# Kernel tuning notes

Hardware: AMD Instinct MI355X
Metric: run time of the kernel (lower is better)

## Reference

```python
import jax, jax.numpy as jnp
import numpy as np

EPS = 1e-12  # matches torch F.normalize default eps

def _l2_normalize(x):
    n = jnp.maximum(jnp.linalg.norm(x, axis=-1, keepdims=True), EPS)
    return x / n

def setup_inputs() -> dict:
    key = jax.random.key(0)
    ks = jax.random.split(key, 6)
    B, H, N, D, E = 4, 12, 4096, 64, 32
    Q = jax.random.normal(ks[0], (B, H, N, D), dtype=jnp.float32)
    K = jax.random.normal(ks[1], (B, H, N, D), dtype=jnp.float32)
    we = jax.random.normal(ks[2], (2, H, D, E), dtype=jnp.float32)
    wr = jax.random.normal(ks[3], (2, H, D, E), dtype=jnp.float32)
    mask = jnp.ones((B, N), dtype=jnp.float32)
    W = jax.random.normal(ks[4], (D, 2 * E), dtype=jnp.float32) * (1.0 / np.sqrt(2 * E))
    b = jnp.zeros((D,), dtype=jnp.float32)
    Lambda = jax.random.uniform(ks[5], (H, E), dtype=jnp.float32)
    return {"Q": Q, "K": K, "we": we, "wr": wr, "mask": mask, "W": W, "b": b, "Lambda": Lambda}

def reference(Q, K, we, wr, mask, W, b, Lambda):
    # feature map: L2 normalize along head_dim
    queries = _l2_normalize(Q)   # [B,H,N,D]
    keys = _l2_normalize(K)      # [B,H,N,D]
    # per-head low-rank projections
    escore = jnp.einsum('bhnd,hde->bhne', queries, we[0])  # [B,H,N,E]
    rscore = jnp.einsum('bhnd,hde->bhne', keys, wr[0])     # [B,H,N,E]
    score = jnp.concatenate([escore, rscore], axis=-1)      # [B,H,N,2E]
    # Linear(2E -> D): score @ W.T + b
    attn_out = jnp.einsum('bhne,de->bhnd', score, W) + b
    attn_out = attn_out * mask[:, None, :, None]
    # trace_no_x = False branch
    return (attn_out, escore, rscore, we[0], wr[0], queries, keys, Lambda)
```

## Files before the change

kernel.cpp:

```cpp
#include <hip/hip_runtime.h>


namespace {
constexpr int Hh = 12;
constexpr int Nn = 4096;
constexpr int Dd = 64;
constexpr int O_ATTN = 0;
constexpr int O_ES   = 12582912;
constexpr int O_RS   = 18874368;
constexpr int O_WE   = 25165824;
constexpr int O_WR   = 25190400;
constexpr int O_Q    = 25214976;
constexpr int O_K    = 37797888;
constexpr int O_LAM  = 50380800;
}

__device__ __forceinline__ int aswz(int d, int r) {
    return d * 128 + (r ^ ((d & 7) << 2));
}

__global__ __launch_bounds__(256, 3)
void pca_fused(const float* __restrict__ Q, const float* __restrict__ Kp,
               const float* __restrict__ we, const float* __restrict__ wr,
               const float* __restrict__ mask, const float* __restrict__ W,
               const float* __restrict__ bias, const float* __restrict__ Lam,
               float* __restrict__ out)
{
    __shared__ float lds[12288];
    float* A  = lds;
    float* Bs = lds + 8192;

    const int tid = threadIdx.x;
    const int bh  = blockIdx.x >> 6;
    const int n0  = (blockIdx.x & 63) << 6;
    const int h   = bh % Hh;
    const int bb  = bh / Hh;

    if (blockIdx.x < 49) {
        int i4 = blockIdx.x * 256 + tid;
        if (i4 < 6144) {
            ((float4*)(out + O_WE))[i4] = ((const float4*)we)[i4];
        } else if (i4 < 12288) {
            ((float4*)(out + O_WR))[i4 - 6144] = ((const float4*)wr)[i4 - 6144];
        } else if (i4 < 12384) {
            ((float4*)(out + O_LAM))[i4 - 12288] = ((const float4*)Lam)[i4 - 12288];
        }
    }

    float wreg[16];
#pragma unroll
    for (int j = 0; j < 16; ++j) wreg[j] = W[tid + 256 * j];

    {
        const float* weh = we + h * 2048;
        const float* wrh = wr + h * 2048;
#pragma unroll
        for (int j = 0; j < 8; ++j) {
            int i = tid + 256 * j;
            int d = i >> 5, e = i & 31;
            Bs[d * 64 + e]      = weh[i];
            Bs[d * 64 + 32 + e] = wrh[i];
        }
    }
    {
        const int rr = tid >> 4;
        const int c4 = (tid & 15) << 2;
#pragma unroll
        for (int p = 0; p < 4; ++p) {
            int r = p * 16 + rr;
            int g = (bh * Nn + n0 + r) * Dd + c4;
            float4 q4 = *(const float4*)(Q + g);
            float4 k4 = *(const float4*)(Kp + g);
            float sq = q4.x*q4.x + q4.y*q4.y + q4.z*q4.z + q4.w*q4.w;
            float sk = k4.x*k4.x + k4.y*k4.y + k4.z*k4.z + k4.w*k4.w;
#pragma unroll
            for (int m = 1; m < 16; m <<= 1) {
                sq += __shfl_xor(sq, m, 64);
                sk += __shfl_xor(sk, m, 64);
            }
            float iq = 1.0f / fmaxf(sqrtf(sq), 1e-12f);
            float ik = 1.0f / fmaxf(sqrtf(sk), 1e-12f);
            q4.x *= iq; q4.y *= iq; q4.z *= iq; q4.w *= iq;
            k4.x *= ik; k4.y *= ik; k4.z *= ik; k4.w *= ik;
            *(float4*)(out + O_Q + g) = q4;
            *(float4*)(out + O_K + g) = k4;
            A[aswz(c4 + 0, r)] = q4.x;  A[aswz(c4 + 0, r) + 64] = k4.x;
            A[aswz(c4 + 1, r)] = q4.y;  A[aswz(c4 + 1, r) + 64] = k4.y;
            A[aswz(c4 + 2, r)] = q4.z;  A[aswz(c4 + 2, r) + 64] = k4.z;
            A[aswz(c4 + 3, r)] = q4.w;  A[aswz(c4 + 3, r) + 64] = k4.w;
        }
    }
    __syncthreads();

    const int tc = tid & 15, tr = tid >> 4;
    const int c0 = tc << 2;
    const int r0 = tr << 2;

    float acc[4][4] = {};
    {
        const int aofs = (tc < 8) ? 0 : 64;
#pragma unroll 8
        for (int k = 0; k < 64; ++k) {
            float4 a4 = *(const float4*)(A + k * 128 + aofs + (r0 ^ ((k & 7) << 2)));
            float4 b4 = *(const float4*)(Bs + k * 64 + c0);
            const float av[4] = {a4.x, a4.y, a4.z, a4.w};
            const float bv[4] = {b4.x, b4.y, b4.z, b4.w};
#pragma unroll
            for (int i = 0; i < 4; ++i)
#pragma unroll
                for (int j = 0; j < 4; ++j)
                    acc[i][j] = fmaf(av[i], bv[j], acc[i][j]);
        }
    }
    {
        float* sb = out + ((tc < 8) ? O_ES : O_RS);
        int ce = (tc & 7) << 2;
#pragma unroll
        for (int i = 0; i < 4; ++i) {
            int o = (bh * Nn + n0 + r0 + i) * 32 + ce;
            *(float4*)(sb + o) = make_float4(acc[i][0], acc[i][1], acc[i][2], acc[i][3]);
        }
    }
    __syncthreads();
#pragma unroll
    for (int j = 0; j < 4; ++j) {
        int c = c0 + j;
        *(float4*)(A + c * 128 + (r0 ^ ((c & 7) << 2))) =
            make_float4(acc[0][j], acc[1][j], acc[2][j], acc[3][j]);
    }
#pragma unroll
    for (int j = 0; j < 16; ++j) {
        int i = tid + 256 * j;
        int d = i >> 6, e = i & 63;
        Bs[e * 64 + (d ^ ((e & 7) << 2))] = wreg[j];
    }
    __syncthreads();

    float acc2[4][4] = {};
#pragma unroll 8
    for (int k = 0; k < 64; ++k) {
        float4 a4 = *(const float4*)(A + k * 128 + (r0 ^ ((k & 7) << 2)));
        float4 b4 = *(const float4*)(Bs + k * 64 + (c0 ^ ((k & 7) << 2)));
        const float av[4] = {a4.x, a4.y, a4.z, a4.w};
        const float bv[4] = {b4.x, b4.y, b4.z, b4.w};
#pragma unroll
        for (int i = 0; i < 4; ++i)
#pragma unroll
            for (int j = 0; j < 4; ++j)
                acc2[i][j] = fmaf(av[i], bv[j], acc2[i][j]);
    }
    float4 b4 = *(const float4*)(bias + c0);
    const float bvv[4] = {b4.x, b4.y, b4.z, b4.w};
#pragma unroll
    for (int i = 0; i < 4; ++i) {
        int n = n0 + r0 + i;
        float mv = mask[bb * Nn + n];
        int o = (bh * Nn + n) * Dd + c0;
        float4 rr;
        rr.x = (acc2[i][0] + bvv[0]) * mv;
        rr.y = (acc2[i][1] + bvv[1]) * mv;
        rr.z = (acc2[i][2] + bvv[2]) * mv;
        rr.w = (acc2[i][3] + bvv[3]) * mv;
        *(float4*)(out + O_ATTN + o) = rr;
    }
}

extern "C" void kernel_launch(void* const* d_in, const int* in_sizes, int n_in,
                              void* d_out, int out_size, void* d_ws, size_t ws_size,
                              hipStream_t stream) {
    const float* Q    = (const float*)d_in[0];
    const float* Kp   = (const float*)d_in[1];
    const float* we   = (const float*)d_in[2];
    const float* wr   = (const float*)d_in[3];
    const float* mask = (const float*)d_in[4];
    const float* W    = (const float*)d_in[5];
    const float* bias = (const float*)d_in[6];
    const float* Lam  = (const float*)d_in[7];
    float* out = (float*)d_out;

    pca_fused<<<dim3(48 * 64), dim3(256), 0, stream>>>(Q, Kp, we, wr, mask, W, bias, Lam, out);
}
```

Measured before the change: 296.9 us.

## Replace fp32 FMA tile GEMMs with bf16 MFMA and compact LDS

Both per-tile matrix products now run on 16x16x32 bf16 MFMA instructions instead of scalar fp32 FMA loops. The projection stage computes escore and rscore, and the output stage applies W. Normalized Q/K, the projection weights and W are rounded to bf16 and stored in XOR-swizzled LDS buffers. This roughly halves shared memory, and launch bounds rise from 3 to 4 blocks per CU. The aim is to cut LDS-read and VALU cost. In exchange, the GEMM inputs lose precision, and outputs are written as scalar stores rather than float4.

```diff
diff --git a/kernel.cpp b/kernel.cpp
--- a/kernel.cpp
+++ b/kernel.cpp
@@ -15,20 +15,31 @@
 constexpr int O_LAM  = 50380800;
 }
 
-__device__ __forceinline__ int aswz(int d, int r) {
-    return d * 128 + (r ^ ((d & 7) << 2));
+typedef float  v4f  __attribute__((ext_vector_type(4)));
+typedef __bf16 v8bf __attribute__((ext_vector_type(8)));
+
+__device__ __forceinline__ unsigned short f2b(float f) {
+    unsigned int x = __float_as_uint(f);
+    x += 0x7fffu + ((x >> 16) & 1u);
+    return (unsigned short)(x >> 16);
 }
 
-__global__ __launch_bounds__(256, 3)
+__device__ __forceinline__ int swz(int row, int k) {
+    return row * 64 + (((k >> 3) ^ (row & 7)) << 3) + (k & 7);
+}
+
+__global__ __launch_bounds__(256, 4)
 void pca_fused(const float* __restrict__ Q, const float* __restrict__ Kp,
                const float* __restrict__ we, const float* __restrict__ wr,
                const float* __restrict__ mask, const float* __restrict__ W,
                const float* __restrict__ bias, const float* __restrict__ Lam,
                float* __restrict__ out)
 {
-    __shared__ float lds[12288];
-    float* A  = lds;
-    float* Bs = lds + 8192;
+    __shared__ __align__(16) unsigned short Qs[4096];
+    __shared__ __align__(16) unsigned short Ks[4096];
+    __shared__ __align__(16) unsigned short WEs[2048];
+    __shared__ __align__(16) unsigned short WRs[2048];
+    __shared__ __align__(16) unsigned short Ws_[4096];
 
     const int tid = threadIdx.x;
     const int bh  = blockIdx.x >> 6;
@@ -47,10 +58,6 @@
         }
     }
 
-    float wreg[16];
-#pragma unroll
-    for (int j = 0; j < 16; ++j) wreg[j] = W[tid + 256 * j];
-
     {
         const float* weh = we + h * 2048;
         const float* wrh = wr + h * 2048;
@@ -58,10 +65,17 @@
         for (int j = 0; j < 8; ++j) {
             int i = tid + 256 * j;
             int d = i >> 5, e = i & 31;
-            Bs[d * 64 + e]      = weh[i];
-            Bs[d * 64 + 32 + e] = wrh[i];
+            WEs[swz(e, d)] = f2b(weh[i]);
+            WRs[swz(e, d)] = f2b(wrh[i]);
+        }
+#pragma unroll
+        for (int j = 0; j < 16; ++j) {
+            int i = tid + 256 * j;
+            int d = i >> 6, e = i & 63;
+            Ws_[swz(d, e)] = f2b(W[i]);
         }
     }
+
     {
         const int rr = tid >> 4;
         const int c4 = (tid & 15) << 2;
@@ -84,84 +98,69 @@
             k4.x *= ik; k4.y *= ik; k4.z *= ik; k4.w *= ik;
             *(float4*)(out + O_Q + g) = q4;
             *(float4*)(out + O_K + g) = k4;
-            A[aswz(c4 + 0, r)] = q4.x;  A[aswz(c4 + 0, r) + 64] = k4.x;
-            A[aswz(c4 + 1, r)] = q4.y;  A[aswz(c4 + 1, r) + 64] = k4.y;
-            A[aswz(c4 + 2, r)] = q4.z;  A[aswz(c4 + 2, r) + 64] = k4.z;
-            A[aswz(c4 + 3, r)] = q4.w;  A[aswz(c4 + 3, r) + 64] = k4.w;
+            int a = swz(r, c4);
+            *(ushort4*)(Qs + a) = make_ushort4(f2b(q4.x), f2b(q4.y), f2b(q4.z), f2b(q4.w));
+            *(ushort4*)(Ks + a) = make_ushort4(f2b(k4.x), f2b(k4.y), f2b(k4.z), f2b(k4.w));
         }
     }
     __syncthreads();
 
-    const int tc = tid & 15, tr = tid >> 4;
-    const int c0 = tc << 2;
-    const int r0 = tr << 2;
+    const int w    = tid >> 6;
+    const int lane = tid & 63;
+    const int quad = lane >> 4;
+    const int n16  = lane & 15;
+    const int m    = w * 16 + n16;
 
-    float acc[4][4] = {};
-    {
-        const int aofs = (tc < 8) ? 0 : 64;
-#pragma unroll 8
-        for (int k = 0; k < 64; ++k) {
-            float4 a4 = *(const float4*)(A + k * 128 + aofs + (r0 ^ ((k & 7) << 2)));
-            float4 b4 = *(const float4*)(Bs + k * 64 + c0);
-            const float av[4] = {a4.x, a4.y, a4.z, a4.w};
-            const float bv[4] = {b4.x, b4.y, b4.z, b4.w};
+    auto ldf = [&](const unsigned short* b, int row, int kb) -> v8bf {
+        return *(const v8bf*)(b + row * 64 + ((((kb << 2) + quad) ^ (row & 7)) << 3));
+    };
+
+    v8bf aq0 = ldf(Qs, m, 0), aq1 = ldf(Qs, m, 1);
+    v8bf ak0 = ldf(Ks, m, 0), ak1 = ldf(Ks, m, 1);
+    v4f accE[2], accR[2];
 #pragma unroll
-            for (int i = 0; i < 4; ++i)
+    for (int nt = 0; nt < 2; ++nt) {
+        int er = nt * 16 + n16;
+        accE[nt] = (v4f){0.f, 0.f, 0.f, 0.f};
+        accR[nt] = (v4f){0.f, 0.f, 0.f, 0.f};
+        accE[nt] = __builtin_amdgcn_mfma_f32_16x16x32_bf16(aq0, ldf(WEs, er, 0), accE[nt], 0, 0, 0);
+        accE[nt] = __builtin_amdgcn_mfma_f32_16x16x32_bf16(aq1, ldf(WEs, er, 1), accE[nt], 0, 0, 0);
+        accR[nt] = __builtin_amdgcn_mfma_f32_16x16x32_bf16(ak0, ldf(WRs, er, 0), accR[nt], 0, 0, 0);
+        accR[nt] = __builtin_amdgcn_mfma_f32_16x16x32_bf16(ak1, ldf(WRs, er, 1), accR[nt], 0, 0, 0);
+    }
+
 #pragma unroll
-                for (int j = 0; j < 4; ++j)
-                    acc[i][j] = fmaf(av[i], bv[j], acc[i][j]);
+    for (int nt = 0; nt < 2; ++nt) {
+#pragma unroll
+        for (int i = 0; i < 4; ++i) {
+            int r = w * 16 + quad * 4 + i;
+            int n = n0 + r;
+            out[O_ES + (bh * Nn + n) * 32 + nt * 16 + n16] = accE[nt][i];
+            out[O_RS + (bh * Nn + n) * 32 + nt * 16 + n16] = accR[nt][i];
+            Qs[swz(r, nt * 16 + n16)]      = f2b(accE[nt][i]);
+            Qs[swz(r, 32 + nt * 16 + n16)] = f2b(accR[nt][i]);
         }
     }
-    {
-        float* sb = out + ((tc < 8) ? O_ES : O_RS);
-        int ce = (tc & 7) << 2;
+
+    v8bf as0 = ldf(Qs, m, 0), as1 = ldf(Qs, m, 1);
+    v4f accD[4];
+#pragma unroll
+    for (int nt = 0; nt < 4; ++nt) {
+        float bv = bias[nt * 16 + n16];
+        accD[nt] = (v4f){bv, bv, bv, bv};
+        accD[nt] = __builtin_amdgcn_mfma_f32_16x16x32_bf16(as0, ldf(Ws_, nt * 16 + n16, 0), accD[nt], 0, 0, 0);
+        accD[nt] = __builtin_amdgcn_mfma_f32_16x16x32_bf16(as1, ldf(Ws_, nt * 16 + n16, 1), accD[nt], 0, 0, 0);
+    }
+    float mv[4];
+#pragma unroll
+    for (int i = 0; i < 4; ++i) mv[i] = mask[bb * Nn + n0 + w * 16 + quad * 4 + i];
+#pragma unroll
+    for (int nt = 0; nt < 4; ++nt) {
 #pragma unroll
         for (int i = 0; i < 4; ++i) {
-            int o = (bh * Nn + n0 + r0 + i) * 32 + ce;
-            *(float4*)(sb + o) = make_float4(acc[i][0], acc[i][1], acc[i][2], acc[i][3]);
+            int n = n0 + w * 16 + quad * 4 + i;
+            out[O_ATTN + (bh * Nn + n) * 64 + nt * 16 + n16] = accD[nt][i] * mv[i];
         }
-    }
-    __syncthreads();
-#pragma unroll
-    for (int j = 0; j < 4; ++j) {
-        int c = c0 + j;
-        *(float4*)(A + c * 128 + (r0 ^ ((c & 7) << 2))) =
-            make_float4(acc[0][j], acc[1][j], acc[2][j], acc[3][j]);
-    }
-#pragma unroll
-    for (int j = 0; j < 16; ++j) {
-        int i = tid + 256 * j;
-        int d = i >> 6, e = i & 63;
-        Bs[e * 64 + (d ^ ((e & 7) << 2))] = wreg[j];
-    }
-    __syncthreads();
-
-    float acc2[4][4] = {};
-#pragma unroll 8
-    for (int k = 0; k < 64; ++k) {
-        float4 a4 = *(const float4*)(A + k * 128 + (r0 ^ ((k & 7) << 2)));
-        float4 b4 = *(const float4*)(Bs + k * 64 + (c0 ^ ((k & 7) << 2)));
-        const float av[4] = {a4.x, a4.y, a4.z, a4.w};
-        const float bv[4] = {b4.x, b4.y, b4.z, b4.w};
-#pragma unroll
-        for (int i = 0; i < 4; ++i)
-#pragma unroll
-            for (int j = 0; j < 4; ++j)
-                acc2[i][j] = fmaf(av[i], bv[j], acc2[i][j]);
-    }
-    float4 b4 = *(const float4*)(bias + c0);
-    const float bvv[4] = {b4.x, b4.y, b4.z, b4.w};
-#pragma unroll
-    for (int i = 0; i < 4; ++i) {
-        int n = n0 + r0 + i;
-        float mv = mask[bb * Nn + n];
-        int o = (bh * Nn + n) * Dd + c0;
-        float4 rr;
-        rr.x = (acc2[i][0] + bvv[0]) * mv;
-        rr.y = (acc2[i][1] + bvv[1]) * mv;
-        rr.z = (acc2[i][2] + bvv[2]) * mv;
-        rr.w = (acc2[i][3] + bvv[3]) * mv;
-        *(float4*)(out + O_ATTN + o) = rr;
     }
 }
 
```

New measurement: 302.0 us. No clear change (+1.7%).
